# Kernel tuning notes

Hardware: AMD Instinct MI355X
Metric: run time of the kernel (lower is better)

Reference implementation:

```python
import jax, jax.numpy as jnp
import numpy as np

SR = 24000          # sample_rate
HOP = 256           # hop_length
K = 1024            # FIR kernel_size = nearest_power_of_two(2.2/50*24000)
RC = 512            # rnn_channels
NF = 4              # n_formants
REV = 24000         # reverb length in samples
L = HOP + K - 1     # per-frame conv output length = 1279
PI = np.pi


def _gru(x, W_ih, W_hh, b_ih, b_hh):
    # x: [B, T, H] -> [B, T, H], torch nn.GRU semantics, h0 = 0
    B = x.shape[0]

    def step(h, xt):
        gi = xt @ W_ih.T + b_ih
        gh = h @ W_hh.T + b_hh
        i_r, i_z, i_n = jnp.split(gi, 3, axis=-1)
        h_r, h_z, h_n = jnp.split(gh, 3, axis=-1)
        r = jax.nn.sigmoid(i_r + h_r)
        zg = jax.nn.sigmoid(i_z + h_z)
        n = jnp.tanh(i_n + r * h_n)
        h = (1.0 - zg) * n + zg * h
        return h, h

    h0 = jnp.zeros((B, RC), x.dtype)
    _, ys = jax.lax.scan(step, h0, jnp.swapaxes(x, 0, 1))
    return jnp.swapaxes(ys, 0, 1)


def setup_inputs() -> dict:
    key = jax.random.key(0)
    ks = jax.random.split(key, 20)
    B, F = 4, 2048
    s = 0.05
    inp = {
        'f0': jax.random.uniform(ks[0], (B, F, 1), minval=100.0, maxval=300.0),
        'loudness': jax.random.normal(ks[1], (B, F, 1)),
        'gender': jax.random.uniform(ks[2], (B, F, 2)),
        'age': jax.random.uniform(ks[3], (B, F, 8)),
        'z': jax.random.normal(ks[4], (B, F, 16)),
        'noise': jax.random.normal(ks[5], (B, F, HOP)),
        'W_in': jax.random.normal(ks[6], (RC, 28)) * s, 'b_in': jnp.zeros((RC,)),
        'W_ih': jax.random.normal(ks[7], (3 * RC, RC)) * s,
        'W_hh': jax.random.normal(ks[8], (3 * RC, RC)) * s,
        'b_ih': jnp.zeros((3 * RC,)), 'b_hh': jnp.zeros((3 * RC,)),
        'W_oq': jax.random.normal(ks[9], (1, RC)) * s, 'b_oq': jnp.zeros((1,)),
        'W_vg': jax.random.normal(ks[10], (1, RC)) * s, 'b_vg': jnp.zeros((1,)),
        'W_ug': jax.random.normal(ks[11], (1, RC)) * s, 'b_ug': jnp.zeros((1,)),
        'W_ff': jax.random.normal(ks[12], (NF, RC)) * s, 'b_ff': jnp.zeros((NF,)),
        'W_fb': jax.random.normal(ks[13], (NF, RC)) * s, 'b_fb': jnp.zeros((NF,)),
        'reverb_ir': jax.random.normal(ks[14], (REV,)) * jnp.exp(-jnp.linspace(0.0, 5.0, REV)),
        'wet_logit': jnp.float32(-1.5),
    }
    return inp


def reference(f0, loudness, gender, age, z, noise,
              W_in, b_in, W_ih, W_hh, b_ih, b_hh,
              W_oq, b_oq, W_vg, b_vg, W_ug, b_ug,
              W_ff, b_ff, W_fb, b_fb, reverb_ir, wet_logit):
    B, F, _ = f0.shape

    # ---- controller ----
    f0c = f0 - jnp.mean(f0, axis=1, keepdims=True)
    inputs = jnp.concatenate([f0c, loudness, gender, age, z], axis=-1)  # [B,F,28]
    x = jax.nn.relu(inputs @ W_in.T + b_in)
    x = _gru(x, W_ih, W_hh, b_ih, b_hh)                                  # [B,F,512]
    oq = jax.nn.sigmoid(x @ W_oq.T + b_oq)                               # [B,F,1]
    v_gain = jax.nn.softplus(x @ W_vg.T + b_vg)
    u_gain = jax.nn.softplus(x @ W_ug.T + b_ug)
    ff = jnp.cumsum(jax.nn.softplus(x @ W_ff.T + b_ff), axis=-1) + 200.0  # [B,F,4]
    fb = jax.nn.softplus(x @ W_fb.T + b_fb) + 50.0

    # ---- Rosenberg glottal source ----
    cycles = f0 * (HOP / SR)                       # [B,F,1]
    cum = jnp.cumsum(cycles, axis=1)
    start = cum - cycles
    start = start - jnp.floor(start)
    ramp = (jnp.arange(HOP, dtype=f0.dtype) / SR)[None, None, :]
    total = start + f0 * ramp                      # [B,F,HOP]
    phi = total - jnp.floor(total)
    eps = 1e-6
    peak = oq * 0.66
    rise = 0.5 * (1.0 - jnp.cos(PI * phi / (peak + eps)))
    fall = jnp.cos(PI * (phi - peak) / (2.0 * (oq - peak) + eps))
    voiced = jnp.where(phi < peak, rise, 0.0)
    voiced = jnp.where((phi >= peak) & (phi < oq), fall, voiced)

    # ---- excitation ----
    excitation = voiced * v_gain + noise * u_gain   # [B,F,HOP]

    # ---- time-varying FIR formant filter ----
    t = jnp.arange(K, dtype=f0.dtype) / SR          # [K]
    ir = jnp.exp(-PI * fb[..., None] * t) * jnp.sin(2.0 * PI * ff[..., None] * t)  # [B,F,4,K]
    combined = jnp.sum(ir, axis=2)                  # [B,F,K]
    scale = jnp.max(jnp.abs(combined), axis=-1, keepdims=True) + 1e-8
    filt = combined / scale
    # torch conv1d is cross-correlation with padding K-1 == full convolution with flipped kernel
    NFFT = 2048  # >= L = 1279, power of two
    Xf = jnp.fft.rfft(excitation, n=NFFT)
    Hf = jnp.fft.rfft(filt[..., ::-1], n=NFFT)
    conv = jnp.fft.irfft(Xf * Hf, n=NFFT)[..., :L]  # [B,F,L]

    # ---- overlap-add (F.fold) ----
    total_len = (F - 1) * HOP + L
    idx = (jnp.arange(F)[:, None] * HOP + jnp.arange(L)[None, :]).reshape(-1)
    audio = jnp.zeros((B, total_len), conv.dtype).at[:, idx].add(conv.reshape(B, -1))

    # ---- FFT reverb ----
    FFTN = 1 << 20  # >= total_len + REV - 1 = 549310
    Af = jnp.fft.rfft(audio, n=FFTN)
    Rf = jnp.fft.rfft(reverb_ir, n=FFTN)
    wetsig = jnp.fft.irfft(Af * Rf[None, :], n=FFTN)[:, :total_len]
    wet = jax.nn.sigmoid(wet_logit)
    out = ((1.0 - wet) * audio + wet * wetsig)[..., None]  # [B,total_len,1]

    return out, oq, v_gain, u_gain, ff, fb
```

## Files before the change

kernel.cpp:

```cpp
#include <hip/hip_runtime.h>
#include <hip/hip_bf16.h>
#include <math.h>

#define PI_F 3.14159265358979323846f
#define TWO_PI_F 6.283185307179586f

constexpr int BB = 4;
constexpr int FF_ = 2048;
constexpr int RC = 512;
constexpr int HOP = 256;
constexpr int KK = 1024;
constexpr int LL = HOP + KK - 1;
constexpr size_t TOT = 525311;
constexpr int APAD = 24064;
constexpr size_t AROW = 549376;
constexpr int REV = 24000;
constexpr size_t AROW2 = 551424;

constexpr size_t O1 = 2101244;
constexpr size_t O2 = 2109436;
constexpr size_t O3 = 2117628;
constexpr size_t O4 = 2125820;
constexpr size_t O5 = 2158588;

constexpr size_t OFF_X      = 0;
constexpr size_t OFF_WTAP   = 8388608;
constexpr size_t OFF_GI     = 16777216;
constexpr size_t OFF_HS     = 67108864;
constexpr size_t OFF_OQ     = 83886080;
constexpr size_t OFF_VG     = 83918848;
constexpr size_t OFF_UG     = 83951616;
constexpr size_t OFF_FFW    = 83984384;
constexpr size_t OFF_FBW    = 84115456;
constexpr size_t OFF_START  = 84246528;
constexpr size_t OFF_F0M    = 84279296;
constexpr size_t OFF_AUDIO  = 92684800;
constexpr size_t OFF_AF16   = OFF_X;

constexpr size_t OFF_HBUF   = OFF_FFW;

__device__ __forceinline__ float softplusf(float x) {
  return x > 20.0f ? x : log1pf(expf(x));
}
__device__ __forceinline__ float sigmoidf_(float x) {
  return 1.0f / (1.0f + expf(-x));
}
__device__ __forceinline__ float fastrcp(float x) {
#if __has_builtin(__builtin_amdgcn_rcpf)
  return __builtin_amdgcn_rcpf(x);
#else
  return 1.0f / x;
#endif
}

typedef _Float16 half2v __attribute__((ext_vector_type(2)));
typedef _Float16 f16x8 __attribute__((ext_vector_type(8)));
typedef float f32x4 __attribute__((ext_vector_type(4)));

__device__ __forceinline__ float dot2f(unsigned wa, unsigned hb, float acc) {
#if __has_builtin(__builtin_amdgcn_fdot2)
  union { unsigned u; half2v h; } A, B;
  A.u = wa; B.u = hb;
  return __builtin_amdgcn_fdot2(A.h, B.h, acc, false);
#else
  union { unsigned u; _Float16 h[2]; } A, B;
  A.u = wa; B.u = hb;
  return fmaf((float)A.h[0], (float)B.h[0], fmaf((float)A.h[1], (float)B.h[1], acc));
#endif
}

__global__ __launch_bounds__(256) void k_f0mean(const float* __restrict__ f0, float* __restrict__ f0m) {
  int b = blockIdx.x, tid = threadIdx.x;
  float s = 0.f;
  for (int t = tid; t < FF_; t += 256) s += f0[b*FF_ + t];
  #pragma unroll
  for (int m = 1; m < 64; m <<= 1) s += __shfl_xor(s, m);
  __shared__ float ws4[4];
  if ((tid & 63) == 0) ws4[tid >> 6] = s;
  __syncthreads();
  if (tid == 0) f0m[b] = (ws4[0] + ws4[1] + ws4[2] + ws4[3]) * (1.0f / 2048.0f);
}

__global__ __launch_bounds__(256) void k_inproj(
    const float* __restrict__ f0, const float* __restrict__ loud,
    const float* __restrict__ gender, const float* __restrict__ age,
    const float* __restrict__ z, const float* __restrict__ f0m,
    const float* __restrict__ Win, const float* __restrict__ bin,
    float* __restrict__ x)
{
  __shared__ float inp[16 * 28];
  int r0 = blockIdx.x * 16;
  int tid = threadIdx.x;
  for (int i = tid; i < 16 * 28; i += 256) {
    int r = i / 28, c = i % 28;
    int bf = r0 + r, b = bf >> 11;
    float v;
    if (c == 0)       v = f0[bf] - f0m[b];
    else if (c == 1)  v = loud[bf];
    else if (c < 4)   v = gender[(size_t)bf*2 + (c - 2)];
    else if (c < 12)  v = age[(size_t)bf*8 + (c - 4)];
    else              v = z[(size_t)bf*16 + (c - 12)];
    inp[i] = v;
  }
  __syncthreads();
  for (int o = tid; o < 16 * 512; o += 256) {
    int r = o >> 9, j = o & 511;
    const float* w = Win + j * 28;
    const float* ip = inp + r * 28;
    float a = bin[j];
    #pragma unroll
    for (int c2 = 0; c2 < 28; ++c2) a = fmaf(w[c2], ip[c2], a);
    x[(size_t)(r0 + r) * 512 + j] = fmaxf(a, 0.0f);
  }
}

__global__ __launch_bounds__(256) void k_gemm_gi(
    const float* __restrict__ A, const float* __restrict__ Bw,
    const float* __restrict__ bias, float* __restrict__ C)
{
  __shared__ unsigned As[64 * 20];
  __shared__ unsigned Bs[64 * 20];
  int tid = threadIdx.x;
  int n0 = blockIdx.x * 64, m0 = blockIdx.y * 64;
  const int w = tid >> 6;
  const int lane = tid & 63;
  const int mrow0 = (w >> 1) * 32;
  const int ncol0 = (w & 1) * 32;
  const int lm = lane & 15;
  const int quad = lane >> 4;

  f32x4 acc00 = {0.f,0.f,0.f,0.f}, acc01 = {0.f,0.f,0.f,0.f};
  f32x4 acc10 = {0.f,0.f,0.f,0.f}, acc11 = {0.f,0.f,0.f,0.f};

  for (int k0 = 0; k0 < 512; k0 += 32) {
    __syncthreads();
    for (int i = tid; i < 1024; i += 256) {
      int r = i >> 4, d = i & 15;
      float2 av = *(const float2*)(A + (size_t)(m0 + r) * 512 + k0 + 2 * d);
      float2 bv = *(const float2*)(Bw + (size_t)(n0 + r) * 512 + k0 + 2 * d);
      union { unsigned u32; _Float16 h[2]; } pa, pb;
      pa.h[0] = (_Float16)av.x; pa.h[1] = (_Float16)av.y;
      pb.h[0] = (_Float16)bv.x; pb.h[1] = (_Float16)bv.y;
      As[r * 20 + d] = pa.u32;
      Bs[r * 20 + d] = pb.u32;
    }
    __syncthreads();
    union { uint4 u; f16x8 h; } a0, a1, b0, b1;
    a0.u = *(const uint4*)&As[(mrow0 + lm) * 20 + quad * 4];
    a1.u = *(const uint4*)&As[(mrow0 + 16 + lm) * 20 + quad * 4];
    b0.u = *(const uint4*)&Bs[(ncol0 + lm) * 20 + quad * 4];
    b1.u = *(const uint4*)&Bs[(ncol0 + 16 + lm) * 20 + quad * 4];
    acc00 = __builtin_amdgcn_mfma_f32_16x16x32_f16(a0.h, b0.h, acc00, 0, 0, 0);
    acc01 = __builtin_amdgcn_mfma_f32_16x16x32_f16(a0.h, b1.h, acc01, 0, 0, 0);
    acc10 = __builtin_amdgcn_mfma_f32_16x16x32_f16(a1.h, b0.h, acc10, 0, 0, 0);
    acc11 = __builtin_amdgcn_mfma_f32_16x16x32_f16(a1.h, b1.h, acc11, 0, 0, 0);
  }
  #pragma unroll
  for (int sm = 0; sm < 2; ++sm) {
    #pragma unroll
    for (int sn = 0; sn < 2; ++sn) {
      const f32x4& ac = sm ? (sn ? acc11 : acc10) : (sn ? acc01 : acc00);
      int col = n0 + ncol0 + sn * 16 + lm;
      float bb = bias[col];
      #pragma unroll
      for (int rg = 0; rg < 4; ++rg) {
        int row = m0 + mrow0 + sm * 16 + quad * 4 + rg;
        C[(size_t)row * 1536 + col] = ac[rg] + bb;
      }
    }
  }
}

__global__ __launch_bounds__(256, 1) void k_gru(
    const float* __restrict__ Whh, const float* __restrict__ bhh,
    const float* __restrict__ gi, float* __restrict__ hs,
    unsigned long long* hbuf,
    const float* __restrict__ f0, float* __restrict__ startw,
    const float* __restrict__ ir, uint4* __restrict__ wtap)
{
  const int tid = threadIdx.x;
  const int bid = blockIdx.x;

  if (bid >= 64) {
    int xb = bid - 64;
    if (xb < 4) {
      __shared__ float ts[256];
      int b = xb;
      const float CY = 256.0f / 24000.0f;
      float c[8], run = 0.f;
      int base = b * 2048 + tid * 8;
      #pragma unroll
      for (int j = 0; j < 8; ++j) { c[j] = run; run += f0[base + j] * CY; }
      ts[tid] = run;
      __syncthreads();
      for (int off = 1; off < 256; off <<= 1) {
        float v = (tid >= off) ? ts[tid - off] : 0.0f;
        __syncthreads();
        ts[tid] += v;
        __syncthreads();
      }
      float excl = (tid == 0) ? 0.0f : ts[tid - 1];
      #pragma unroll
      for (int j = 0; j < 8; ++j) {
        float st = excl + c[j];
        startw[base + j] = st - floorf(st);
      }
    } else {
      int g = (xb - 4) * 256 + tid;
      int p = g >> 6, l = g & 63;
      if (p < 752) {
        int base = 32 * p + 16 + (l & 15) - ((l >> 4) << 3);
        unsigned dw[4];
        #pragma unroll
        for (int j = 0; j < 4; ++j) {
          int i0 = base - 2 * j, i1 = base - 2 * j - 1;
          float v0 = (i0 >= 0 && i0 < REV) ? ir[i0] : 0.0f;
          float v1 = (i1 >= 0 && i1 < REV) ? ir[i1] : 0.0f;
          union { unsigned u32; _Float16 h[2]; } pk;
          pk.h[0] = (_Float16)v0; pk.h[1] = (_Float16)v1;
          dw[j] = pk.u32;
        }
        uint4 o; o.x = dw[0]; o.y = dw[1]; o.z = dw[2]; o.w = dw[3];
        wtap[(size_t)(p << 6) + l] = o;
      }
    }
    return;
  }

  __shared__ unsigned hs2[2][292];
  __shared__ float red[2][384];
  __shared__ float bhh_s[96];

  const int b   = (bid & 7) >> 1;
  const int wgi = ((bid >> 3) << 1) | (bid & 1);
  const int u0  = wgi * 32;
  const int piece = tid & 3;
  const int rp    = tid >> 2;

  unsigned w0r[64], w1r[64];
  if (tid < 192) {
    int r0 = 2 * rp, r1 = 2 * rp + 1;
    const float* s0 = Whh + (size_t)((r0 >> 5) * 512 + u0 + (r0 & 31)) * 512 + piece * 128;
    const float* s1 = Whh + (size_t)((r1 >> 5) * 512 + u0 + (r1 & 31)) * 512 + piece * 128;
    #pragma unroll
    for (int j = 0; j < 64; ++j) {
      float2 a = *(const float2*)(s0 + 2 * j);
      float2 c = *(const float2*)(s1 + 2 * j);
      union { unsigned u32; _Float16 hh[2]; } ca, cb;
      ca.hh[0] = (_Float16)a.x; ca.hh[1] = (_Float16)a.y;
      cb.hh[0] = (_Float16)c.x; cb.hh[1] = (_Float16)c.y;
      w0r[j] = ca.u32; w1r[j] = cb.u32;
    }
  } else {
    #pragma unroll
    for (int j = 0; j < 64; ++j) { w0r[j] = 0u; w1r[j] = 0u; }
  }
  if (tid < 96) bhh_s[tid] = bhh[(tid >> 5) * 512 + u0 + (tid & 31)];
  __syncthreads();

  float hprev = 0.0f;

  #pragma unroll 1
  for (unsigned t = 0; t < 2048; ++t) {
    const int p = (int)(t & 1u);
    float gir = 0.f, giz = 0.f, gin = 0.f;
    if (tid < 32) {
      const float* gp = gi + (size_t)(b * 2048 + (int)t) * 1536 + u0 + tid;
      gir = gp[0]; giz = gp[512]; gin = gp[1024];
    }
    {
      const unsigned long long* pp = hbuf + ((size_t)p * 4 + b) * 256 + tid;
      unsigned long long w = __hip_atomic_load(pp, __ATOMIC_RELAXED, __HIP_MEMORY_SCOPE_AGENT);
      while ((unsigned)(w >> 32) != t)
        w = __hip_atomic_load(pp, __ATOMIC_RELAXED, __HIP_MEMORY_SCOPE_AGENT);
      hs2[p][(tid >> 5) * 36 + (tid & 31)] = (unsigned)w;
    }
    __syncthreads();
    if (tid < 192) {
      const unsigned* hp0 = &hs2[p][(2 * piece) * 36];
      const unsigned* hp1 = &hs2[p][(2 * piece + 1) * 36];
      float a00 = 0.f, a01 = 0.f, a10 = 0.f, a11 = 0.f;
      #pragma unroll
      for (int i = 0; i < 8; ++i) {
        uint4 h4 = *(const uint4*)(hp0 + 4 * i);
        a00 = dot2f(w0r[4 * i + 0], h4.x, a00);
        a01 = dot2f(w0r[4 * i + 1], h4.y, a01);
        a00 = dot2f(w0r[4 * i + 2], h4.z, a00);
        a01 = dot2f(w0r[4 * i + 3], h4.w, a01);
        a10 = dot2f(w1r[4 * i + 0], h4.x, a10);
        a11 = dot2f(w1r[4 * i + 1], h4.y, a11);
        a10 = dot2f(w1r[4 * i + 2], h4.z, a10);
        a11 = dot2f(w1r[4 * i + 3], h4.w, a11);
      }
      #pragma unroll
      for (int i = 0; i < 8; ++i) {
        uint4 h4 = *(const uint4*)(hp1 + 4 * i);
        a00 = dot2f(w0r[32 + 4 * i + 0], h4.x, a00);
        a01 = dot2f(w0r[32 + 4 * i + 1], h4.y, a01);
        a00 = dot2f(w0r[32 + 4 * i + 2], h4.z, a00);
        a01 = dot2f(w0r[32 + 4 * i + 3], h4.w, a01);
        a10 = dot2f(w1r[32 + 4 * i + 0], h4.x, a10);
        a11 = dot2f(w1r[32 + 4 * i + 1], h4.y, a11);
        a10 = dot2f(w1r[32 + 4 * i + 2], h4.z, a10);
        a11 = dot2f(w1r[32 + 4 * i + 3], h4.w, a11);
      }
      red[p][(2 * rp) * 4 + piece]     = a00 + a01;
      red[p][(2 * rp + 1) * 4 + piece] = a10 + a11;
    }
    __syncthreads();
    if (tid < 32) {
      float4 q0 = *(const float4*)&red[p][tid * 4];
      float4 z0 = *(const float4*)&red[p][(32 + tid) * 4];
      float4 n0 = *(const float4*)&red[p][(64 + tid) * 4];
      float ghr = ((q0.x + q0.y) + (q0.z + q0.w)) + bhh_s[tid];
      float ghz = ((z0.x + z0.y) + (z0.z + z0.w)) + bhh_s[32 + tid];
      float ghn = ((n0.x + n0.y) + (n0.z + n0.w)) + bhh_s[64 + tid];
      float r  = fastrcp(1.0f + __expf(-(gir + ghr)));
      float zg = fastrcp(1.0f + __expf(-(giz + ghz)));
      float e2 = __expf(2.0f * (gin + r * ghn));
      float n  = 1.0f - 2.0f * fastrcp(e2 + 1.0f);
      float hnew = (1.0f - zg) * n + zg * hprev;
      hprev = hnew;
      float hpart = __shfl_xor(hnew, 1);
      if ((tid & 1) == 0) {
        union { unsigned u32; _Float16 hh[2]; } pk;
        pk.hh[0] = (_Float16)hnew;
        pk.hh[1] = (_Float16)hpart;
        unsigned long long wq = ((unsigned long long)(t + 1u) << 32) | (unsigned long long)pk.u32;
        __hip_atomic_store(hbuf + ((size_t)((t + 1u) & 1u) * 4 + b) * 256 + (u0 >> 1) + (tid >> 1),
                           wq, __ATOMIC_RELAXED, __HIP_MEMORY_SCOPE_AGENT);
      }
      hs[(size_t)(b * 2048 + (int)t) * 512 + u0 + tid] = hnew;
    }
  }
}

__global__ __launch_bounds__(256) void k_heads(
    const float* __restrict__ hs,
    const float* __restrict__ Woq, const float* __restrict__ boq,
    const float* __restrict__ Wvg, const float* __restrict__ bvg,
    const float* __restrict__ Wug, const float* __restrict__ bug,
    const float* __restrict__ Wff, const float* __restrict__ bff,
    const float* __restrict__ Wfb, const float* __restrict__ bfb,
    float* __restrict__ out,
    float* __restrict__ oqw, float* __restrict__ vgw, float* __restrict__ ugw,
    float* __restrict__ ffw, float* __restrict__ fbw)
{
  int bf = blockIdx.x, tid = threadIdx.x;
  const float* h = hs + (size_t)bf * 512;
  float p[11];
  #pragma unroll
  for (int i = 0; i < 11; ++i) p[i] = 0.f;
  for (int k = tid; k < 512; k += 256) {
    float hv = h[k];
    p[0] = fmaf(Woq[k], hv, p[0]);
    p[1] = fmaf(Wvg[k], hv, p[1]);
    p[2] = fmaf(Wug[k], hv, p[2]);
    p[3] = fmaf(Wff[k], hv, p[3]);
    p[4] = fmaf(Wff[512 + k], hv, p[4]);
    p[5] = fmaf(Wff[1024 + k], hv, p[5]);
    p[6] = fmaf(Wff[1536 + k], hv, p[6]);
    p[7] = fmaf(Wfb[k], hv, p[7]);
    p[8] = fmaf(Wfb[512 + k], hv, p[8]);
    p[9] = fmaf(Wfb[1024 + k], hv, p[9]);
    p[10] = fmaf(Wfb[1536 + k], hv, p[10]);
  }
  #pragma unroll
  for (int i = 0; i < 11; ++i) {
    float v = p[i];
    #pragma unroll
    for (int m = 1; m < 64; m <<= 1) v += __shfl_xor(v, m);
    p[i] = v;
  }
  __shared__ float r4[4][11];
  if ((tid & 63) == 0) {
    int w = tid >> 6;
    #pragma unroll
    for (int i = 0; i < 11; ++i) r4[w][i] = p[i];
  }
  __syncthreads();
  if (tid == 0) {
    float s[11];
    #pragma unroll
    for (int i = 0; i < 11; ++i) s[i] = r4[0][i] + r4[1][i] + r4[2][i] + r4[3][i];
    float oqv = sigmoidf_(s[0] + boq[0]);
    float vg = softplusf(s[1] + bvg[0]);
    float ug = softplusf(s[2] + bug[0]);
    out[O1 + bf] = oqv; oqw[bf] = oqv;
    out[O2 + bf] = vg;  vgw[bf] = vg;
    out[O3 + bf] = ug;  ugw[bf] = ug;
    float run = 200.0f;
    #pragma unroll
    for (int j = 0; j < 4; ++j) {
      run += softplusf(s[3 + j] + bff[j]);
      out[O4 + (size_t)bf * 4 + j] = run; ffw[(size_t)bf * 4 + j] = run;
    }
    #pragma unroll
    for (int j = 0; j < 4; ++j) {
      float g = softplusf(s[7 + j] + bfb[j]) + 50.0f;
      out[O5 + (size_t)bf * 4 + j] = g; fbw[(size_t)bf * 4 + j] = g;
    }
  }
}

__global__ __launch_bounds__(256) void k_synth(
    const float* __restrict__ f0, const float* __restrict__ noise,
    const float* __restrict__ startw, const float* __restrict__ oqw,
    const float* __restrict__ vgw, const float* __restrict__ ugw,
    const float* __restrict__ ffw, const float* __restrict__ fbw,
    float* __restrict__ audio)
{
  __shared__ float es[256];
  __shared__ float fp[1536];
  __shared__ float ffs[4], fbs[4], ssc[1], wmax[4];
  int bf = blockIdx.x, tid = threadIdx.x;
  int b = bf >> 11, f = bf & 2047;

  {
    float st = startw[bf], f0v = f0[bf], oqv = oqw[bf], vg = vgw[bf], ug = ugw[bf];
    float total = st + f0v * ((float)tid * (1.0f / 24000.0f));
    float phi = total - floorf(total);
    float peak = oqv * 0.66f;
    float rise = 0.5f * (1.0f - __cosf(PI_F * phi / (peak + 1e-6f)));
    float fall = __cosf(PI_F * (phi - peak) / (2.0f * (oqv - peak) + 1e-6f));
    float v = (phi < peak) ? rise : ((phi < oqv) ? fall : 0.0f);
    es[tid] = v * vg + noise[(size_t)bf * 256 + tid] * ug;
  }
  if (tid < 4) { ffs[tid] = ffw[(size_t)bf * 4 + tid]; fbs[tid] = fbw[(size_t)bf * 4 + tid]; }
  fp[tid] = 0.0f;
  fp[1280 + tid] = 0.0f;
  __syncthreads();

  float vals[4];
  float am = 0.f;
  #pragma unroll
  for (int it = 0; it < 4; ++it) {
    int k = it * 256 + tid;
    float t = (float)k * (1.0f / 24000.0f);
    float s = 0.f;
    #pragma unroll
    for (int j = 0; j < 4; ++j)
      s += __expf(-PI_F * fbs[j] * t) * __sinf(TWO_PI_F * ffs[j] * t);
    vals[it] = s;
    am = fmaxf(am, fabsf(s));
  }
  #pragma unroll
  for (int m = 1; m < 64; m <<= 1) am = fmaxf(am, __shfl_xor(am, m));
  if ((tid & 63) == 0) wmax[tid >> 6] = am;
  __syncthreads();
  if (tid == 0) ssc[0] = fmaxf(fmaxf(wmax[0], wmax[1]), fmaxf(wmax[2], wmax[3])) + 1e-8f;
  __syncthreads();
  float inv = 1.0f / ssc[0];
  #pragma unroll
  for (int it = 0; it < 4; ++it) {
    int k = it * 256 + tid;
    fp[256 + (1023 - k)] = vals[it] * inv;
  }
  __syncthreads();

  int n0 = tid * 5;
  float V0 = fp[n0 + 256], V1 = fp[n0 + 257], V2 = fp[n0 + 258], V3 = fp[n0 + 259], V4 = fp[n0 + 260];
  float a0 = 0.f, a1 = 0.f, a2 = 0.f, a3 = 0.f, a4 = 0.f;
  #pragma unroll 4
  for (int m = 0; m < 256; ++m) {
    float e = es[m];
    a0 = fmaf(e, V0, a0); a1 = fmaf(e, V1, a1); a2 = fmaf(e, V2, a2);
    a3 = fmaf(e, V3, a3); a4 = fmaf(e, V4, a4);
    V4 = V3; V3 = V2; V2 = V1; V1 = V0;
    V0 = fp[n0 + 255 - m];
  }
  float* arow = audio + (size_t)b * AROW + APAD + (size_t)f * 256;
  if (n0 + 0 < LL) atomicAdd(&arow[n0 + 0], a0);
  if (n0 + 1 < LL) atomicAdd(&arow[n0 + 1], a1);
  if (n0 + 2 < LL) atomicAdd(&arow[n0 + 2], a2);
  if (n0 + 3 < LL) atomicAdd(&arow[n0 + 3], a3);
  if (n0 + 4 < LL) atomicAdd(&arow[n0 + 4], a4);
}

__global__ __launch_bounds__(256) void k_packaudio(const float* __restrict__ audio,
                                                   unsigned* __restrict__ af) {
  int idx = blockIdx.x * 256 + threadIdx.x;
  int b = blockIdx.y;
  size_t i0 = (size_t)idx * 2;
  if (i0 < AROW2) {
    float a = (i0 < AROW)     ? audio[(size_t)b * AROW + i0]     : 0.0f;
    float c = (i0 + 1 < AROW) ? audio[(size_t)b * AROW + i0 + 1] : 0.0f;
    union { unsigned u32; _Float16 h[2]; } pk;
    pk.h[0] = (_Float16)a; pk.h[1] = (_Float16)c;
    af[(size_t)b * (AROW2 / 2) + idx] = pk.u32;
  }
}

constexpr int PC = 16;
constexpr int NCHUNK = 47;
constexpr int WINH = 2544;

__global__ __launch_bounds__(256) void k_reverb(
    const float* __restrict__ audio, const unsigned short* __restrict__ af,
    const uint4* __restrict__ wtap, const float* __restrict__ wetl,
    float* __restrict__ out)
{
  __shared__ __align__(16) unsigned short win[WINH];
  __shared__ uint4 wlds[PC * 64];
  int tb = blockIdx.x, b = blockIdx.y, tid = threadIdx.x;
  const int wv = tid >> 6, lane = tid & 63;
  const int lm = lane & 15, quad = lane >> 4;
  int q0 = tb * 128;
  const unsigned short* afrow = af + (size_t)b * AROW2;
  f32x4 acc0 = {0.f,0.f,0.f,0.f}, acc1 = {0.f,0.f,0.f,0.f};

  for (int c = 0; c < NCHUNK; ++c) {
    int p0 = c * PC;
    int b_lo = 16 * q0 - 32 * (p0 + PC - 1) - 16;
    const uint4* src = (const uint4*)(afrow + (APAD + b_lo));
    __syncthreads();
    for (int u = tid; u < 318 + PC * 64; u += 256) {
      if (u < 318) ((uint4*)win)[u] = src[u];
      else         wlds[u - 318] = wtap[(size_t)p0 * 64 + (u - 318)];
    }
    __syncthreads();
    int offb = 16 * lm + 8 * quad;
    int tA = (2 * wv) * 256 + offb, tB = (2 * wv + 1) * 256 + offb;
    #pragma unroll 4
    for (int pl = 0; pl < PC; ++pl) {
      union { uint4 u; f16x8 h; } wf, b0, b1;
      wf.u = wlds[pl * 64 + lane];
      int offp = 32 * (PC - 1 - pl);
      b0.u = *(const uint4*)&win[offp + tA];
      b1.u = *(const uint4*)&win[offp + tB];
      acc0 = __builtin_amdgcn_mfma_f32_16x16x32_f16(wf.h, b0.h, acc0, 0, 0, 0);
      acc1 = __builtin_amdgcn_mfma_f32_16x16x32_f16(wf.h, b1.h, acc1, 0, 0, 0);
    }
  }
  float wet = sigmoidf_(wetl[0]);
  const float* arow = audio + (size_t)b * AROW;
  #pragma unroll
  for (int tile = 0; tile < 2; ++tile) {
    const f32x4& ac = tile ? acc1 : acc0;
    int qt = q0 + (2 * wv + tile) * 16 + lm;
    #pragma unroll
    for (int rg = 0; rg < 4; ++rg) {
      long t = (long)16 * qt + quad * 4 + rg;
      if (t < (long)TOT) {
        float av = arow[APAD + t];
        out[(size_t)b * TOT + t] = (1.0f - wet) * av + wet * ac[rg];
      }
    }
  }
}

extern "C" void kernel_launch(void* const* d_in, const int* in_sizes, int n_in,
                              void* d_out, int out_size, void* d_ws, size_t ws_size,
                              hipStream_t stream) {
  const float* f0       = (const float*)d_in[0];
  const float* loud     = (const float*)d_in[1];
  const float* gender   = (const float*)d_in[2];
  const float* age      = (const float*)d_in[3];
  const float* z        = (const float*)d_in[4];
  const float* noise    = (const float*)d_in[5];
  const float* W_in     = (const float*)d_in[6];
  const float* b_in     = (const float*)d_in[7];
  const float* W_ih     = (const float*)d_in[8];
  const float* W_hh     = (const float*)d_in[9];
  const float* b_ih     = (const float*)d_in[10];
  const float* b_hh     = (const float*)d_in[11];
  const float* W_oq     = (const float*)d_in[12];
  const float* b_oq     = (const float*)d_in[13];
  const float* W_vg     = (const float*)d_in[14];
  const float* b_vg     = (const float*)d_in[15];
  const float* W_ug     = (const float*)d_in[16];
  const float* b_ug     = (const float*)d_in[17];
  const float* W_ff     = (const float*)d_in[18];
  const float* b_ff     = (const float*)d_in[19];
  const float* W_fb     = (const float*)d_in[20];
  const float* b_fb     = (const float*)d_in[21];
  const float* rev_ir   = (const float*)d_in[22];
  const float* wet_l    = (const float*)d_in[23];

  float* out = (float*)d_out;
  char* ws = (char*)d_ws;
  float* x      = (float*)(ws + OFF_X);
  float* gi     = (float*)(ws + OFF_GI);
  float* hs     = (float*)(ws + OFF_HS);
  float* oqw    = (float*)(ws + OFF_OQ);
  float* vgw    = (float*)(ws + OFF_VG);
  float* ugw    = (float*)(ws + OFF_UG);
  float* ffw    = (float*)(ws + OFF_FFW);
  float* fbw    = (float*)(ws + OFF_FBW);
  float* startw = (float*)(ws + OFF_START);
  float* f0m    = (float*)(ws + OFF_F0M);
  unsigned long long* hbuf = (unsigned long long*)(ws + OFF_HBUF);
  uint4* wtap   = (uint4*)(ws + OFF_WTAP);
  unsigned* af  = (unsigned*)(ws + OFF_AF16);
  float* audio  = (float*)(ws + OFF_AUDIO);

  hipMemsetAsync(ws + OFF_HBUF, 0, 16384, stream);
  hipMemsetAsync(ws + OFF_AUDIO, 0, (size_t)4 * AROW * 4, stream);

  k_f0mean<<<4, 256, 0, stream>>>(f0, f0m);
  k_inproj<<<512, 256, 0, stream>>>(f0, loud, gender, age, z, f0m, W_in, b_in, x);
  k_gemm_gi<<<dim3(24, 128), 256, 0, stream>>>(x, W_ih, b_ih, gi);
  k_gru<<<256, 256, 0, stream>>>(W_hh, b_hh, gi, hs, hbuf,
                                 f0, startw, rev_ir, wtap);
  k_heads<<<8192, 256, 0, stream>>>(hs, W_oq, b_oq, W_vg, b_vg, W_ug, b_ug,
                                    W_ff, b_ff, W_fb, b_fb, out, oqw, vgw, ugw, ffw, fbw);
  k_synth<<<8192, 256, 0, stream>>>(f0, noise, startw, oqw, vgw, ugw, ffw, fbw, audio);
  k_packaudio<<<dim3(1077, 4), 256, 0, stream>>>(audio, af);
  k_reverb<<<dim3(257, 4), 256, 0, stream>>>(audio, (const unsigned short*)af, wtap, wet_l, out);
}
```

Baseline: 3.209 ms.

## Share reverb tap tiles across all four batch rows in one block

The reverb kernel now has each block handle all four batch rows. It stages four audio windows in LDS and reuses each loaded reverb-tap fragment for eight MFMAs instead of two. This removes three quarters of the global and LDS loads of the tap weights. The trade-off is a grid shrunk from 1028 to 257 blocks, which on a many-CU GPU may leave compute units idle, plus more accumulator registers and more LDS per block.

```diff
diff --git a/kernel.cpp b/kernel.cpp
--- a/kernel.cpp
+++ b/kernel.cpp
@@ -500,50 +500,73 @@
     const uint4* __restrict__ wtap, const float* __restrict__ wetl,
     float* __restrict__ out)
 {
-  __shared__ __align__(16) unsigned short win[WINH];
+  __shared__ __align__(16) unsigned short win[4 * WINH];
   __shared__ uint4 wlds[PC * 64];
-  int tb = blockIdx.x, b = blockIdx.y, tid = threadIdx.x;
+  int tb = blockIdx.x, tid = threadIdx.x;
   const int wv = tid >> 6, lane = tid & 63;
   const int lm = lane & 15, quad = lane >> 4;
   int q0 = tb * 128;
-  const unsigned short* afrow = af + (size_t)b * AROW2;
-  f32x4 acc0 = {0.f,0.f,0.f,0.f}, acc1 = {0.f,0.f,0.f,0.f};
+  f32x4 accA0 = {0.f,0.f,0.f,0.f}, accA1 = {0.f,0.f,0.f,0.f};
+  f32x4 accA2 = {0.f,0.f,0.f,0.f}, accA3 = {0.f,0.f,0.f,0.f};
+  f32x4 accB0 = {0.f,0.f,0.f,0.f}, accB1 = {0.f,0.f,0.f,0.f};
+  f32x4 accB2 = {0.f,0.f,0.f,0.f}, accB3 = {0.f,0.f,0.f,0.f};
 
   for (int c = 0; c < NCHUNK; ++c) {
     int p0 = c * PC;
     int b_lo = 16 * q0 - 32 * (p0 + PC - 1) - 16;
-    const uint4* src = (const uint4*)(afrow + (APAD + b_lo));
     __syncthreads();
-    for (int u = tid; u < 318 + PC * 64; u += 256) {
-      if (u < 318) ((uint4*)win)[u] = src[u];
-      else         wlds[u - 318] = wtap[(size_t)p0 * 64 + (u - 318)];
+    for (int u = tid; u < 4 * 318 + PC * 64; u += 256) {
+      if (u < 4 * 318) {
+        int bb = u / 318, i = u - bb * 318;
+        const uint4* src = (const uint4*)(af + (size_t)bb * AROW2 + (APAD + b_lo));
+        ((uint4*)win)[bb * 318 + i] = src[i];
+      } else {
+        wlds[u - 4 * 318] = wtap[(size_t)p0 * 64 + (u - 4 * 318)];
+      }
     }
     __syncthreads();
     int offb = 16 * lm + 8 * quad;
     int tA = (2 * wv) * 256 + offb, tB = (2 * wv + 1) * 256 + offb;
-    #pragma unroll 4
+    #pragma unroll 2
     for (int pl = 0; pl < PC; ++pl) {
       union { uint4 u; f16x8 h; } wf, b0, b1;
       wf.u = wlds[pl * 64 + lane];
       int offp = 32 * (PC - 1 - pl);
-      b0.u = *(const uint4*)&win[offp + tA];
-      b1.u = *(const uint4*)&win[offp + tB];
-      acc0 = __builtin_amdgcn_mfma_f32_16x16x32_f16(wf.h, b0.h, acc0, 0, 0, 0);
-      acc1 = __builtin_amdgcn_mfma_f32_16x16x32_f16(wf.h, b1.h, acc1, 0, 0, 0);
+      b0.u = *(const uint4*)&win[0 * WINH + offp + tA];
+      b1.u = *(const uint4*)&win[0 * WINH + offp + tB];
+      accA0 = __builtin_amdgcn_mfma_f32_16x16x32_f16(wf.h, b0.h, accA0, 0, 0, 0);
+      accB0 = __builtin_amdgcn_mfma_f32_16x16x32_f16(wf.h, b1.h, accB0, 0, 0, 0);
+      b0.u = *(const uint4*)&win[1 * WINH + offp + tA];
+      b1.u = *(const uint4*)&win[1 * WINH + offp + tB];
+      accA1 = __builtin_amdgcn_mfma_f32_16x16x32_f16(wf.h, b0.h, accA1, 0, 0, 0);
+      accB1 = __builtin_amdgcn_mfma_f32_16x16x32_f16(wf.h, b1.h, accB1, 0, 0, 0);
+      b0.u = *(const uint4*)&win[2 * WINH + offp + tA];
+      b1.u = *(const uint4*)&win[2 * WINH + offp + tB];
+      accA2 = __builtin_amdgcn_mfma_f32_16x16x32_f16(wf.h, b0.h, accA2, 0, 0, 0);
+      accB2 = __builtin_amdgcn_mfma_f32_16x16x32_f16(wf.h, b1.h, accB2, 0, 0, 0);
+      b0.u = *(const uint4*)&win[3 * WINH + offp + tA];
+      b1.u = *(const uint4*)&win[3 * WINH + offp + tB];
+      accA3 = __builtin_amdgcn_mfma_f32_16x16x32_f16(wf.h, b0.h, accA3, 0, 0, 0);
+      accB3 = __builtin_amdgcn_mfma_f32_16x16x32_f16(wf.h, b1.h, accB3, 0, 0, 0);
     }
   }
   float wet = sigmoidf_(wetl[0]);
-  const float* arow = audio + (size_t)b * AROW;
-  #pragma unroll
-  for (int tile = 0; tile < 2; ++tile) {
-    const f32x4& ac = tile ? acc1 : acc0;
-    int qt = q0 + (2 * wv + tile) * 16 + lm;
-    #pragma unroll
-    for (int rg = 0; rg < 4; ++rg) {
-      long t = (long)16 * qt + quad * 4 + rg;
-      if (t < (long)TOT) {
-        float av = arow[APAD + t];
-        out[(size_t)b * TOT + t] = (1.0f - wet) * av + wet * ac[rg];
+  #pragma unroll
+  for (int bb = 0; bb < 4; ++bb) {
+    const f32x4& acA = bb == 0 ? accA0 : bb == 1 ? accA1 : bb == 2 ? accA2 : accA3;
+    const f32x4& acB = bb == 0 ? accB0 : bb == 1 ? accB1 : bb == 2 ? accB2 : accB3;
+    const float* arow = audio + (size_t)bb * AROW;
+    #pragma unroll
+    for (int tile = 0; tile < 2; ++tile) {
+      const f32x4& ac = tile ? acB : acA;
+      int qt = q0 + (2 * wv + tile) * 16 + lm;
+      #pragma unroll
+      for (int rg = 0; rg < 4; ++rg) {
+        long t = (long)16 * qt + quad * 4 + rg;
+        if (t < (long)TOT) {
+          float av = arow[APAD + t];
+          out[(size_t)bb * TOT + t] = (1.0f - wet) * av + wet * ac[rg];
+        }
       }
     }
   }
@@ -606,5 +629,5 @@
                                     W_ff, b_ff, W_fb, b_fb, out, oqw, vgw, ugw, ffw, fbw);
   k_synth<<<8192, 256, 0, stream>>>(f0, noise, startw, oqw, vgw, ugw, ffw, fbw, audio);
   k_packaudio<<<dim3(1077, 4), 256, 0, stream>>>(audio, af);
-  k_reverb<<<dim3(257, 4), 256, 0, stream>>>(audio, (const unsigned short*)af, wtap, wet_l, out);
-}
+  k_reverb<<<257, 256, 0, stream>>>(audio, (const unsigned short*)af, wtap, wet_l, out);
+}
```

Result: slower. 3.287 ms (+2.4%).
